# Kernel optimization log

Hardware: AMD Instinct MI355X
Metric: run time of the kernel (lower is better)

## Reference

```python
import jax, jax.numpy as jnp
import numpy as np

D = 768
H = 12
DH = D // H
PAIRS4 = [(0, 1), (0, 2), (0, 3), (1, 2), (1, 3), (2, 3)]
J6 = jnp.array([[0,0,0,0,0,1],[0,0,0,0,-1,0],[0,0,0,1,0,0],[0,0,1,0,0,0],[0,-1,0,0,0,0],[1,0,0,0,0,0]], dtype=jnp.float32)


def exterior(p1, p2):
    # p1,p2: (..., 4) -> normalized Plucker coords (..., 6)
    parts = [p1[..., i] * p2[..., j] - p1[..., j] * p2[..., i] for i, j in PAIRS4]
    L = jnp.stack(parts, axis=-1)
    n = jnp.clip(jnp.linalg.norm(L, axis=-1, keepdims=True), 1e-12)
    return L / n


def layernorm(x, g, b, eps=1e-5):
    m = jnp.mean(x, axis=-1, keepdims=True)
    v = jnp.var(x, axis=-1, keepdims=True)
    return (x - m) * jax.lax.rsqrt(v + eps) * g + b


def setup_inputs() -> dict:
    key = jax.random.key(0)
    ks = jax.random.split(key, 16)
    s = 0.02
    inp = {
        'x': jax.random.normal(ks[0], (1, 2048, D), dtype=jnp.float32),
        'ln1_g': jnp.ones((D,), jnp.float32), 'ln1_b': jnp.zeros((D,), jnp.float32),
        'qkv_w': jax.random.normal(ks[1], (D, 3 * D), jnp.float32) * s,
        'qkv_b': jnp.zeros((3 * D,), jnp.float32),
        'w1_write': jax.random.normal(ks[2], (D, 4 * H), jnp.float32) * s,
        'w2_write': jax.random.normal(ks[3], (D, 4 * H), jnp.float32) * s,
        'w1_read': jax.random.normal(ks[4], (D, 4 * H), jnp.float32) * s,
        'w2_read': jax.random.normal(ks[5], (D, 4 * H), jnp.float32) * s,
        'geo_v_w': jax.random.normal(ks[6], (D, D), jnp.float32) * s,
        'geo_v_b': jnp.zeros((D,), jnp.float32),
        'gate_w': jax.random.normal(ks[7], (D, H), jnp.float32) * s,
        'gate_b': jnp.zeros((H,), jnp.float32),
        'inc_scale': jnp.ones((H,), jnp.float32),
        'out_w': jax.random.normal(ks[8], (D, D), jnp.float32) * s,
        'out_b': jnp.zeros((D,), jnp.float32),
        'ln2_g': jnp.ones((D,), jnp.float32), 'ln2_b': jnp.zeros((D,), jnp.float32),
        'fc_w': jax.random.normal(ks[9], (D, 4 * D), jnp.float32) * s,
        'fc_b': jnp.zeros((4 * D,), jnp.float32),
        'proj_w': jax.random.normal(ks[10], (4 * D, D), jnp.float32) * s,
        'proj_b': jnp.zeros((D,), jnp.float32),
    }
    return inp


def dual_path_attention(x, qkv_w, qkv_b, w1_write, w2_write, w1_read, w2_read,
                        geo_v_w, geo_v_b, gate_w, gate_b, inc_scale, out_w, out_b):
    B, T, _ = x.shape
    scale = DH ** -0.5
    qkv = (x @ qkv_w + qkv_b).reshape(B, T, 3, H, DH)
    q = qkv[:, :, 0].transpose(0, 2, 1, 3)  # (B,H,T,dh)
    k = qkv[:, :, 1].transpose(0, 2, 1, 3)
    v = qkv[:, :, 2].transpose(0, 2, 1, 3)
    std_logits = jnp.einsum('bhtd,bhsd->bhts', q, k) * scale

    x_prev = jnp.concatenate([jnp.zeros((B, 1, x.shape[-1]), x.dtype), x[:, :-1]], axis=1)
    w1 = (x_prev @ w1_write).reshape(B, T, H, 4)
    w2 = (x @ w2_write).reshape(B, T, H, 4)
    write_lines = exterior(w1, w2)  # (B,T,H,6)
    r1 = (x @ w1_read).reshape(B, T, H, 4)
    r2 = (x @ w2_read).reshape(B, T, H, 4)
    read_lines = exterior(r1, r2)
    J_write = jnp.einsum('bthi,ij->bthj', write_lines, J6)
    geo_logits = jnp.einsum('bthp,bshp->bhts', read_lines, J_write)
    geo_logits = geo_logits * inc_scale[None, :, None, None]

    mask = jnp.triu(jnp.ones((T, T), dtype=bool), k=1)  # True above diagonal
    neg = jnp.finfo(x.dtype).min
    std_attn = jax.nn.softmax(jnp.where(mask, neg, std_logits), axis=-1)
    std_out = jnp.einsum('bhts,bhsd->bthd', std_attn, v).reshape(B, T, -1)
    geo_attn = jax.nn.softmax(jnp.where(mask, neg, geo_logits), axis=-1)
    geo_v = (x @ geo_v_w + geo_v_b).reshape(B, T, H, DH).transpose(0, 2, 1, 3)
    geo_out = jnp.einsum('bhts,bhsd->bthd', geo_attn, geo_v).reshape(B, T, -1)

    gate = jax.nn.sigmoid(x @ gate_w + gate_b).mean(axis=-1, keepdims=True)
    combined = (1 - gate) * std_out + gate * geo_out
    return combined @ out_w + out_b


def reference(x, ln1_g, ln1_b, qkv_w, qkv_b, w1_write, w2_write, w1_read, w2_read,
              geo_v_w, geo_v_b, gate_w, gate_b, inc_scale, out_w, out_b,
              ln2_g, ln2_b, fc_w, fc_b, proj_w, proj_b):
    h = x + dual_path_attention(layernorm(x, ln1_g, ln1_b), qkv_w, qkv_b,
                                w1_write, w2_write, w1_read, w2_read,
                                geo_v_w, geo_v_b, gate_w, gate_b, inc_scale,
                                out_w, out_b)
    m = layernorm(h, ln2_g, ln2_b)
    mlp = jax.nn.gelu(m @ fc_w + fc_b) @ proj_w + proj_b
    return h + mlp
```

## Files before the change

kernel.cpp:

```cpp
#include <hip/hip_runtime.h>
#include <hip/hip_bf16.h>
#include <math.h>

#define TT 2048
#define DD 768

typedef __bf16 bf16x8 __attribute__((ext_vector_type(8)));
typedef float f32x4 __attribute__((ext_vector_type(4)));

__device__ __forceinline__ void gload16(const void* g, void* l) {
    __builtin_amdgcn_global_load_lds(
        (const __attribute__((address_space(1))) unsigned int*)g,
        (__attribute__((address_space(3))) unsigned int*)l, 16, 0, 0);
}

__device__ __forceinline__ bf16x8 zero8() {
    bf16x8 v;
    #pragma unroll
    for (int j = 0; j < 8; ++j) v[j] = (__bf16)0.0f;
    return v;
}

__global__ __launch_bounds__(256) void ln_kernel(const float* __restrict__ in,
    const float* __restrict__ g, const float* __restrict__ b,
    __hip_bfloat16* __restrict__ out)
{
    const int t = blockIdx.x;
    const int tid = threadIdx.x;
    const float* row = in + (size_t)t * DD;
    float x0 = row[tid], x1 = row[tid + 256], x2 = row[tid + 512];
    float s = x0 + x1 + x2;
    float q = x0 * x0 + x1 * x1 + x2 * x2;
    #pragma unroll
    for (int m = 1; m < 64; m <<= 1) {
        s += __shfl_xor(s, m);
        q += __shfl_xor(q, m);
    }
    __shared__ float ssum[4], sqsum[4];
    const int w = tid >> 6;
    if ((tid & 63) == 0) { ssum[w] = s; sqsum[w] = q; }
    __syncthreads();
    s = ssum[0] + ssum[1] + ssum[2] + ssum[3];
    q = sqsum[0] + sqsum[1] + sqsum[2] + sqsum[3];
    const float mean = s * (1.0f / DD);
    const float var = q * (1.0f / DD) - mean * mean;
    const float rs = rsqrtf(var + 1e-5f);
    __hip_bfloat16* orow = out + (size_t)t * DD;
    orow[tid]       = __float2bfloat16((x0 - mean) * rs * g[tid]       + b[tid]);
    orow[tid + 256] = __float2bfloat16((x1 - mean) * rs * g[tid + 256] + b[tid + 256]);
    orow[tid + 512] = __float2bfloat16((x2 - mean) * rs * g[tid + 512] + b[tid + 512]);
}

__global__ __launch_bounds__(256) void castT_kernel(const float* __restrict__ in,
    __hip_bfloat16* __restrict__ out, int K, int N)
{
    __shared__ float t[32][33];
    const int n0 = blockIdx.x << 5, k0 = blockIdx.y << 5;
    const int tx = threadIdx.x & 31, ty = threadIdx.x >> 5;
    #pragma unroll
    for (int i = 0; i < 32; i += 8)
        t[ty + i][tx] = in[(size_t)(k0 + ty + i) * N + n0 + tx];
    __syncthreads();
    #pragma unroll
    for (int i = 0; i < 32; i += 8)
        out[(size_t)(n0 + ty + i) * K + k0 + tx] = __float2bfloat16(t[tx][ty + i]);
}

__device__ __forceinline__ float gelu_f(float x) {
    float u = 0.7978845608028654f * (x + 0.044715f * x * x * x);
    return 0.5f * x * (1.0f + tanhf(u));
}

__global__ __launch_bounds__(256) void mgemm64_kernel(
    const __hip_bfloat16* __restrict__ A, const __hip_bfloat16* __restrict__ Bt,
    const float* __restrict__ bias, const float* __restrict__ resid,
    void* __restrict__ Cout, float* __restrict__ Pb0, float* __restrict__ Pb1,
    int M, int N, int K, int kz, int epi, int omode)
{
    __shared__ __hip_bfloat16 As[64 * 32];
    __shared__ __hip_bfloat16 Bs[128 * 32];
    const int tid = threadIdx.x;
    const int lane = tid & 63, w = tid >> 6;
    const int colBase = blockIdx.x << 7, rowBase = blockIdx.y << 6;
    const int z = blockIdx.z;
    const int Kc = K / kz, koff = z * Kc;

    const int lr = lane >> 2, pc = lane & 3;
    const int n = lane & 15, quad = lane >> 4;

    const int arow = (w << 4) + lr;
    const int ac = (pc ^ ((arow >> 1) & 3)) << 3;
    const int brow0 = (w << 5) + lr, brow1 = brow0 + 16;
    const int bc0 = (pc ^ ((brow0 >> 1) & 3)) << 3;
    const int bc1 = (pc ^ ((brow1 >> 1) & 3)) << 3;

    f32x4 acc[8];
    #pragma unroll
    for (int j = 0; j < 8; ++j) acc[j] = (f32x4){0.f, 0.f, 0.f, 0.f};

    const int arF = (w << 4) + n;
    const int aposF = (quad ^ ((arF >> 1) & 3)) << 3;

    for (int kk = koff; kk < koff + Kc; kk += 32) {
        __syncthreads();
        gload16(A  + (size_t)(rowBase + arow) * K + kk + ac,   &As[(w << 4) * 32]);
        gload16(Bt + (size_t)(colBase + brow0) * K + kk + bc0, &Bs[(w << 5) * 32]);
        gload16(Bt + (size_t)(colBase + brow1) * K + kk + bc1, &Bs[((w << 5) + 16) * 32]);
        __syncthreads();

        bf16x8 af = *(const bf16x8*)&As[arF * 32 + aposF];
        #pragma unroll
        for (int j = 0; j < 8; ++j) {
            const int rb = (j << 4) + n;
            bf16x8 bfj = *(const bf16x8*)&Bs[rb * 32 + ((quad ^ ((rb >> 1) & 3)) << 3)];
            acc[j] = __builtin_amdgcn_mfma_f32_16x16x32_bf16(af, bfj, acc[j], 0, 0, 0);
        }
    }

    if (kz == 1) {
        #pragma unroll
        for (int j = 0; j < 8; ++j) {
            const int col = colBase + (j << 4) + n;
            const float bj = bias[col];
            #pragma unroll
            for (int r = 0; r < 4; ++r) {
                const int row = rowBase + (w << 4) + (quad << 2) + r;
                float v = acc[j][r] + bj;
                if (epi == 1) v = gelu_f(v);
                else if (epi == 2) v += resid[(size_t)row * N + col];
                if (omode == 1) ((__hip_bfloat16*)Cout)[(size_t)row * N + col] = __float2bfloat16(v);
                else ((float*)Cout)[(size_t)row * N + col] = v;
            }
        }
    } else {
        float* P = (z == 0) ? Pb0 : Pb1;
        #pragma unroll
        for (int j = 0; j < 8; ++j) {
            const int col = colBase + (j << 4) + n;
            #pragma unroll
            for (int r = 0; r < 4; ++r) {
                const int row = rowBase + (w << 4) + (quad << 2) + r;
                P[(size_t)row * N + col] = acc[j][r];
            }
        }
    }
}

__global__ __launch_bounds__(256) void kred_kernel(
    const float* __restrict__ p0, const float* __restrict__ p1,
    const float* __restrict__ bias, const float* __restrict__ resid,
    float* __restrict__ out, int N)
{
    const int base = (blockIdx.x * 256 + threadIdx.x) << 2;
    float4 a = *(const float4*)&p0[base];
    float4 b = *(const float4*)&p1[base];
    float4 bi = *(const float4*)&bias[base % N];
    float4 rs = *(const float4*)&resid[base];
    float4 o;
    o.x = a.x + b.x + bi.x + rs.x;
    o.y = a.y + b.y + bi.y + rs.y;
    o.z = a.z + b.z + bi.z + rs.z;
    o.w = a.w + b.w + bi.w + rs.w;
    *(float4*)&out[base] = o;
}

__device__ __forceinline__ void exterior6(const float* a, const float* b, float* L) {
    L[0] = a[0] * b[1] - a[1] * b[0];
    L[1] = a[0] * b[2] - a[2] * b[0];
    L[2] = a[0] * b[3] - a[3] * b[0];
    L[3] = a[1] * b[2] - a[2] * b[1];
    L[4] = a[1] * b[3] - a[3] * b[1];
    L[5] = a[2] * b[3] - a[3] * b[2];
    float n = sqrtf(L[0]*L[0] + L[1]*L[1] + L[2]*L[2] + L[3]*L[3] + L[4]*L[4] + L[5]*L[5]);
    float inv = 1.f / fmaxf(n, 1e-12f);
    #pragma unroll
    for (int p = 0; p < 6; ++p) L[p] *= inv;
}

__global__ __launch_bounds__(256) void smallproj_kernel(
    const __hip_bfloat16* __restrict__ ln1,
    const float* __restrict__ w1w, const float* __restrict__ w2w,
    const float* __restrict__ w1r, const float* __restrict__ w2r,
    const float* __restrict__ gw, const float* __restrict__ gb,
    __hip_bfloat16* __restrict__ rlb, __hip_bfloat16* __restrict__ jwb,
    float* __restrict__ gate)
{
    const int t = blockIdx.x;
    const int tid = threadIdx.x;
    __shared__ float xc[768], xp[768], res[204];
    const __hip_bfloat16* cur = ln1 + (size_t)t * DD;
    #pragma unroll
    for (int i = 0; i < 3; ++i) {
        int idx = tid + (i << 8);
        xc[idx] = __bfloat162float(cur[idx]);
        xp[idx] = (t > 0) ? __bfloat162float(cur[idx - DD]) : 0.f;
    }
    __syncthreads();
    if (tid < 204) {
        const float* wsel; const float* xv; int col, stride;
        if (tid < 48)       { wsel = w2w; xv = xc; col = tid;       stride = 48; }
        else if (tid < 96)  { wsel = w1w; xv = xp; col = tid - 48;  stride = 48; }
        else if (tid < 144) { wsel = w1r; xv = xc; col = tid - 96;  stride = 48; }
        else if (tid < 192) { wsel = w2r; xv = xc; col = tid - 144; stride = 48; }
        else                { wsel = gw;  xv = xc; col = tid - 192; stride = 12; }
        float s = 0.f;
        for (int k = 0; k < 768; ++k) s += xv[k] * wsel[(size_t)k * stride + col];
        if (tid >= 192) s += gb[col];
        res[tid] = s;
    }
    __syncthreads();
    if (tid < 12) {
        const int h = tid;
        float a[4], b[4], L[6];
        #pragma unroll
        for (int i = 0; i < 4; ++i) { a[i] = res[48 + h * 4 + i]; b[i] = res[h * 4 + i]; }
        exterior6(a, b, L);
        __hip_bfloat16* jwp = jwb + (size_t)h * 16384 + t * 8;
        jwp[0] = __float2bfloat16( L[5]); jwp[1] = __float2bfloat16(-L[4]);
        jwp[2] = __float2bfloat16( L[3]); jwp[3] = __float2bfloat16( L[2]);
        jwp[4] = __float2bfloat16(-L[1]); jwp[5] = __float2bfloat16( L[0]);
        jwp[6] = __float2bfloat16(0.f);   jwp[7] = __float2bfloat16(0.f);
        #pragma unroll
        for (int i = 0; i < 4; ++i) { a[i] = res[96 + h * 4 + i]; b[i] = res[144 + h * 4 + i]; }
        exterior6(a, b, L);
        __hip_bfloat16* rlp = rlb + (size_t)h * 16384 + t * 8;
        #pragma unroll
        for (int p = 0; p < 6; ++p) rlp[p] = __float2bfloat16(L[p]);
        rlp[6] = __float2bfloat16(0.f); rlp[7] = __float2bfloat16(0.f);
    }
    if (tid == 0) {
        float g = 0.f;
        #pragma unroll
        for (int i = 0; i < 12; ++i) g += 1.f / (1.f + __expf(-res[192 + i]));
        gate[t] = g * (1.f / 12.f);
    }
}

__global__ __launch_bounds__(256) void vt_kernel(
    const __hip_bfloat16* __restrict__ qkvB, const __hip_bfloat16* __restrict__ geovB,
    __hip_bfloat16* __restrict__ VT, __hip_bfloat16* __restrict__ GVT)
{
    __shared__ __hip_bfloat16 tile[64][72];
    const int s0 = blockIdx.x << 6, h = blockIdx.y;
    const bool isGV = (blockIdx.z != 0);
    const __hip_bfloat16* src = isGV ? (geovB + h * 64) : (qkvB + 1536 + h * 64);
    const int stride = isGV ? 768 : 2304;
    __hip_bfloat16* dst = (isGV ? GVT : VT) + (size_t)h * 131072;
    const int tid = threadIdx.x;
    const int r = tid >> 2, c = (tid & 3) << 3;
    *(bf16x8*)&tile[r][c]      = *(const bf16x8*)&src[(size_t)(s0 + r) * stride + c];
    *(bf16x8*)&tile[r][c + 32] = *(const bf16x8*)&src[(size_t)(s0 + r) * stride + c + 32];
    __syncthreads();
    __hip_bfloat16 tmp[8];
    #pragma unroll
    for (int j = 0; j < 8; ++j) tmp[j] = tile[c + j][r];
    *(bf16x8*)&dst[(size_t)r * 2048 + s0 + c] = *(const bf16x8*)tmp;
    #pragma unroll
    for (int j = 0; j < 8; ++j) tmp[j] = tile[c + 32 + j][r];
    *(bf16x8*)&dst[(size_t)r * 2048 + s0 + c + 32] = *(const bf16x8*)tmp;
}

__global__ __launch_bounds__(256) void mattn_kernel(
    const __hip_bfloat16* __restrict__ qkvB, const __hip_bfloat16* __restrict__ VT,
    const __hip_bfloat16* __restrict__ GVT, const __hip_bfloat16* __restrict__ rlb,
    const __hip_bfloat16* __restrict__ jwb, const float* __restrict__ gate,
    const float* __restrict__ inc_scale, __hip_bfloat16* __restrict__ comb,
    __hip_bfloat16* __restrict__ Opart, float* __restrict__ stats)
{
    __shared__ __hip_bfloat16 Ks0[2048], Ks1[2048];
    __shared__ __hip_bfloat16 VTs0[2048], VTs1[2048];
    __shared__ __hip_bfloat16 GVTs0[2048], GVTs1[2048];
    __shared__ __hip_bfloat16 JWs[64][8];
    __shared__ __bf16 Ps[64][72];
    __shared__ __bf16 Pg[64][72];

    const int j = 59 - blockIdx.x;
    const int hh = blockIdx.y;
    int qt, c, nc;
    if (j < 12)      { qt = j; c = 0; nc = 1; }
    else if (j < 36) { int t2 = j - 12; qt = 12 + (t2 >> 1); c = t2 & 1; nc = 2; }
    else             { int t2 = j - 36; int d3 = t2 / 3; qt = 24 + d3; c = t2 - d3 * 3; nc = 3; }
    const int q0 = qt << 6;
    const int nk = qt + 1;
    const int ktb = c * nk / nc;
    const int kte = (c + 1) * nk / nc - 1;
    const int tid = threadIdx.x;
    const int w = tid >> 6, lane = tid & 63;
    const int n = lane & 15, quad = lane >> 4;

    const int qrow = q0 + (w << 4) + n;
    const size_t qb = (size_t)qrow * 2304 + hh * 64;
    bf16x8 af0 = *(const bf16x8*)&qkvB[qb + (quad << 3)];
    bf16x8 af1 = *(const bf16x8*)&qkvB[qb + 32 + (quad << 3)];
    bf16x8 rlA = zero8();
    if (quad == 0) rlA = *(const bf16x8*)&rlb[(size_t)hh * 16384 + (size_t)qrow * 8];
    const float isc = inc_scale[hh];
    const float mgc = fabsf(isc);
    const size_t vbase = (size_t)hh * 131072;

    const int sRow = tid >> 2, sc = tid & 3;
    const int sPos = ((sc ^ ((sRow >> 1) & 3)) << 3);
    const int sOff = sc << 3;

    f32x4 Os[4], Og[4];
    float m_s[4], lsp[4], lgp[4];
    #pragma unroll
    for (int r = 0; r < 4; ++r) {
        m_s[r] = -1e30f; lsp[r] = 0.f; lgp[r] = 0.f;
        Os[r] = (f32x4){0.f, 0.f, 0.f, 0.f};
        Og[r] = (f32x4){0.f, 0.f, 0.f, 0.f};
    }

    bf16x8 rK0, rK1, rV0, rV1, rG0, rG1, rJ = zero8();
    {
        const int k0 = ktb << 6;
        const size_t kb = (size_t)(k0 + sRow) * 2304 + 768 + hh * 64;
        const size_t vb = vbase + (size_t)sRow * 2048 + k0;
        rK0 = *(const bf16x8*)&qkvB[kb + sOff];
        rK1 = *(const bf16x8*)&qkvB[kb + sOff + 32];
        rV0 = *(const bf16x8*)&VT[vb + sOff];
        rV1 = *(const bf16x8*)&VT[vb + sOff + 32];
        rG0 = *(const bf16x8*)&GVT[vb + sOff];
        rG1 = *(const bf16x8*)&GVT[vb + sOff + 32];
        if (tid < 64) rJ = *(const bf16x8*)&jwb[(size_t)hh * 16384 + (size_t)(k0 + tid) * 8];
    }

    for (int kt = ktb; kt <= kte; ++kt) {
        const int k0 = kt << 6;
        __syncthreads();
        *(bf16x8*)&Ks0[sRow * 32 + sPos]  = rK0;
        *(bf16x8*)&Ks1[sRow * 32 + sPos]  = rK1;
        *(bf16x8*)&VTs0[sRow * 32 + sPos] = rV0;
        *(bf16x8*)&VTs1[sRow * 32 + sPos] = rV1;
        *(bf16x8*)&GVTs0[sRow * 32 + sPos] = rG0;
        *(bf16x8*)&GVTs1[sRow * 32 + sPos] = rG1;
        if (tid < 64) *(bf16x8*)&JWs[tid][0] = rJ;
        if (kt < kte) {
            const int k1 = (kt + 1) << 6;
            const size_t kb = (size_t)(k1 + sRow) * 2304 + 768 + hh * 64;
            const size_t vb = vbase + (size_t)sRow * 2048 + k1;
            rK0 = *(const bf16x8*)&qkvB[kb + sOff];
            rK1 = *(const bf16x8*)&qkvB[kb + sOff + 32];
            rV0 = *(const bf16x8*)&VT[vb + sOff];
            rV1 = *(const bf16x8*)&VT[vb + sOff + 32];
            rG0 = *(const bf16x8*)&GVT[vb + sOff];
            rG1 = *(const bf16x8*)&GVT[vb + sOff + 32];
            if (tid < 64) rJ = *(const bf16x8*)&jwb[(size_t)hh * 16384 + (size_t)(k1 + tid) * 8];
        }
        __syncthreads();

        f32x4 Ss[4], Sg[4];
        #pragma unroll
        for (int t = 0; t < 4; ++t) {
            Ss[t] = (f32x4){0.f, 0.f, 0.f, 0.f};
            Sg[t] = (f32x4){0.f, 0.f, 0.f, 0.f};
        }
        #pragma unroll
        for (int t = 0; t < 4; ++t) {
            const int krow = (t << 4) + n;
            const int kpos = ((quad ^ ((krow >> 1) & 3)) << 3);
            bf16x8 kb0 = *(const bf16x8*)&Ks0[krow * 32 + kpos];
            bf16x8 kb1 = *(const bf16x8*)&Ks1[krow * 32 + kpos];
            Ss[t] = __builtin_amdgcn_mfma_f32_16x16x32_bf16(af0, kb0, Ss[t], 0, 0, 0);
            Ss[t] = __builtin_amdgcn_mfma_f32_16x16x32_bf16(af1, kb1, Ss[t], 0, 0, 0);
            bf16x8 jb = zero8();
            if (quad == 0) jb = *(const bf16x8*)&JWs[krow][0];
            Sg[t] = __builtin_amdgcn_mfma_f32_16x16x32_bf16(rlA, jb, Sg[t], 0, 0, 0);
        }
        #pragma unroll
        for (int t = 0; t < 4; ++t) {
            #pragma unroll
            for (int r = 0; r < 4; ++r) { Ss[t][r] *= 0.125f; Sg[t][r] *= isc; }
        }
        if (kt == qt) {
            #pragma unroll
            for (int t = 0; t < 4; ++t) {
                const int sg = k0 + (t << 4) + n;
                #pragma unroll
                for (int r = 0; r < 4; ++r) {
                    const int qg = q0 + (w << 4) + (quad << 2) + r;
                    if (sg > qg) { Ss[t][r] = -1e30f; Sg[t][r] = -1e30f; }
                }
            }
        }

        #pragma unroll
        for (int r = 0; r < 4; ++r) {
            float mx = fmaxf(fmaxf(Ss[0][r], Ss[1][r]), fmaxf(Ss[2][r], Ss[3][r]));
            #pragma unroll
            for (int mk = 1; mk < 16; mk <<= 1) mx = fmaxf(mx, __shfl_xor(mx, mk));
            float mnew = fmaxf(m_s[r], mx);
            float alpha = __expf(m_s[r] - mnew);
            m_s[r] = mnew;
            float sm = 0.f;
            #pragma unroll
            for (int t = 0; t < 4; ++t) { Ss[t][r] = __expf(Ss[t][r] - mnew); sm += Ss[t][r]; }
            lsp[r] = lsp[r] * alpha + sm;
            #pragma unroll
            for (int t = 0; t < 4; ++t) Os[t][r] *= alpha;

            float smg = 0.f;
            #pragma unroll
            for (int t = 0; t < 4; ++t) { Sg[t][r] = __expf(Sg[t][r] - mgc); smg += Sg[t][r]; }
            lgp[r] += smg;
        }

        #pragma unroll
        for (int t = 0; t < 4; ++t) {
            #pragma unroll
            for (int r = 0; r < 4; ++r) {
                Ps[(w << 4) + (quad << 2) + r][(t << 4) + n] = (__bf16)Ss[t][r];
                Pg[(w << 4) + (quad << 2) + r][(t << 4) + n] = (__bf16)Sg[t][r];
            }
        }
        asm volatile("s_waitcnt lgkmcnt(0)" ::: "memory");

        #pragma unroll
        for (int st = 0; st < 2; ++st) {
            bf16x8 ap = *(const bf16x8*)&Ps[(w << 4) + n][(st << 5) + (quad << 3)];
            bf16x8 gp = *(const bf16x8*)&Pg[(w << 4) + n][(st << 5) + (quad << 3)];
            const __hip_bfloat16* Vh = st ? VTs1 : VTs0;
            const __hip_bfloat16* Gh = st ? GVTs1 : GVTs0;
            #pragma unroll
            for (int dt = 0; dt < 4; ++dt) {
                const int vrow = (dt << 4) + n;
                const int vpos = ((quad ^ ((vrow >> 1) & 3)) << 3);
                bf16x8 vb2 = *(const bf16x8*)&Vh[vrow * 32 + vpos];
                bf16x8 gb2 = *(const bf16x8*)&Gh[vrow * 32 + vpos];
                Os[dt] = __builtin_amdgcn_mfma_f32_16x16x32_bf16(ap, vb2, Os[dt], 0, 0, 0);
                Og[dt] = __builtin_amdgcn_mfma_f32_16x16x32_bf16(gp, gb2, Og[dt], 0, 0, 0);
            }
        }
    }

    float l_s[4], l_g[4];
    #pragma unroll
    for (int r = 0; r < 4; ++r) {
        float ls = lsp[r], lg = lgp[r];
        #pragma unroll
        for (int mk = 1; mk < 16; mk <<= 1) {
            ls += __shfl_xor(ls, mk);
            lg += __shfl_xor(lg, mk);
        }
        l_s[r] = ls; l_g[r] = lg;
    }

    if (nc == 1) {
        #pragma unroll
        for (int r = 0; r < 4; ++r) {
            const int row = q0 + (w << 4) + (quad << 2) + r;
            const float g = gate[row];
            const float invs = (1.f - g) / l_s[r], invg = g / l_g[r];
            #pragma unroll
            for (int dt = 0; dt < 4; ++dt) {
                float val = Os[dt][r] * invs + Og[dt][r] * invg;
                comb[(size_t)row * DD + hh * 64 + (dt << 4) + n] = __float2bfloat16(val);
            }
        }
    } else {
        const int base = (qt < 24) ? ((qt - 12) << 1) : (24 + (qt - 24) * 3);
        const int slot = hh * 48 + base + c;
        __hip_bfloat16* op = Opart + (size_t)slot * 8192;
        float* st = stats + (size_t)slot * 256;
        #pragma unroll
        for (int r = 0; r < 4; ++r) {
            const int rloc = (w << 4) + (quad << 2) + r;
            #pragma unroll
            for (int dt = 0; dt < 4; ++dt) {
                const int col = (dt << 4) + n;
                op[rloc * 128 + col]      = __float2bfloat16(Os[dt][r]);
                op[rloc * 128 + 64 + col] = __float2bfloat16(Og[dt][r]);
            }
            if (n == 0) {
                st[rloc * 4 + 0] = m_s[r]; st[rloc * 4 + 1] = l_s[r];
                st[rloc * 4 + 2] = mgc;    st[rloc * 4 + 3] = l_g[r];
            }
        }
    }
}

__global__ __launch_bounds__(256) void acomb_kernel(
    const __hip_bfloat16* __restrict__ Opart, const float* __restrict__ stats,
    const float* __restrict__ gate, __hip_bfloat16* __restrict__ comb)
{
    const int qt = 12 + blockIdx.x;
    const int h = blockIdx.y;
    const int nc = (qt < 24) ? 2 : 3;
    const int sb = h * 48 + ((qt < 24) ? ((qt - 12) << 1) : (24 + (qt - 24) * 3));
    const int tid = threadIdx.x;
    const int rloc = tid >> 2;
    const int cseg = (tid & 3) << 4;
    const int row = (qt << 6) + rloc;
    float ms = -1e30f, mg = -1e30f;
    for (int c = 0; c < nc; ++c) {
        const float* st = stats + (size_t)(sb + c) * 256 + rloc * 4;
        ms = fmaxf(ms, st[0]);
        mg = fmaxf(mg, st[2]);
    }
    float wsc[3], wgc[3];
    float ls = 0.f, lg = 0.f;
    for (int c = 0; c < nc; ++c) {
        const float* st = stats + (size_t)(sb + c) * 256 + rloc * 4;
        wsc[c] = __expf(st[0] - ms); ls += st[1] * wsc[c];
        wgc[c] = __expf(st[2] - mg); lg += st[3] * wgc[c];
    }
    const float g = gate[row];
    const float fs = (1.f - g) / ls, fg = g / lg;
    #pragma unroll
    for (int cc = 0; cc < 16; ++cc) {
        const int col = cseg + cc;
        float os = 0.f, og = 0.f;
        for (int c = 0; c < nc; ++c) {
            const __hip_bfloat16* op = Opart + (size_t)(sb + c) * 8192 + rloc * 128;
            os += __bfloat162float(op[col]) * wsc[c];
            og += __bfloat162float(op[64 + col]) * wgc[c];
        }
        comb[(size_t)row * DD + h * 64 + col] = __float2bfloat16(os * fs + og * fg);
    }
}

extern "C" void kernel_launch(void* const* d_in, const int* in_sizes, int n_in,
                              void* d_out, int out_size, void* d_ws, size_t ws_size,
                              hipStream_t stream) {
    (void)in_sizes; (void)n_in; (void)out_size; (void)ws_size;
    const float* x      = (const float*)d_in[0];
    const float* ln1_g  = (const float*)d_in[1];
    const float* ln1_b  = (const float*)d_in[2];
    const float* qkv_w  = (const float*)d_in[3];
    const float* qkv_b  = (const float*)d_in[4];
    const float* w1w    = (const float*)d_in[5];
    const float* w2w    = (const float*)d_in[6];
    const float* w1r    = (const float*)d_in[7];
    const float* w2r    = (const float*)d_in[8];
    const float* gvw    = (const float*)d_in[9];
    const float* gvb    = (const float*)d_in[10];
    const float* gw     = (const float*)d_in[11];
    const float* gb     = (const float*)d_in[12];
    const float* isc    = (const float*)d_in[13];
    const float* ow     = (const float*)d_in[14];
    const float* ob     = (const float*)d_in[15];
    const float* ln2_g  = (const float*)d_in[16];
    const float* ln2_b  = (const float*)d_in[17];
    const float* fcw    = (const float*)d_in[18];
    const float* fcb    = (const float*)d_in[19];
    const float* pw     = (const float*)d_in[20];
    const float* pb     = (const float*)d_in[21];
    float* out = (float*)d_out;
    char* wsb  = (char*)d_ws;

    __hip_bfloat16* qkvB  = (__hip_bfloat16*)(wsb + 0);
    __hip_bfloat16* geovB = (__hip_bfloat16*)(wsb + 9437184);
    __hip_bfloat16* VTb   = (__hip_bfloat16*)(wsb + 12582912);
    __hip_bfloat16* GVTb  = (__hip_bfloat16*)(wsb + 15728640);
    __hip_bfloat16* rlb   = (__hip_bfloat16*)(wsb + 18874368);
    __hip_bfloat16* jwb   = (__hip_bfloat16*)(wsb + 19267584);
    float*          gate  = (float*)(wsb + 19660800);
    __hip_bfloat16* ln1   = (__hip_bfloat16*)(wsb + 19668992);
    __hip_bfloat16* comb  = (__hip_bfloat16*)(wsb + 22814720);
    float*          hbuf  = (float*)(wsb + 25960448);
    __hip_bfloat16* qkvwt = (__hip_bfloat16*)(wsb + 32251904);
    __hip_bfloat16* gvwt  = (__hip_bfloat16*)(wsb + 35790848);
    __hip_bfloat16* owt   = (__hip_bfloat16*)(wsb + 36970496);
    float*          stats = (float*)(wsb + 38150144);
    __hip_bfloat16* Opart = (__hip_bfloat16*)hbuf;
    __hip_bfloat16* fcwt  = qkvwt;
    __hip_bfloat16* pwt   = (__hip_bfloat16*)(wsb + 0);
    __hip_bfloat16* fcact = (__hip_bfloat16*)(wsb + 4718592);
    float* Ppart0 = (float*)(wsb + 18874368);
    float* Ppart1 = (float*)(wsb + 32251904);

    castT_kernel<<<dim3(72, 24), 256, 0, stream>>>(qkv_w, qkvwt, 768, 2304);
    castT_kernel<<<dim3(24, 24), 256, 0, stream>>>(gvw, gvwt, 768, 768);
    ln_kernel<<<TT, 256, 0, stream>>>(x, ln1_g, ln1_b, ln1);
    mgemm64_kernel<<<dim3(18, 32, 1), 256, 0, stream>>>(ln1, qkvwt, qkv_b, nullptr, qkvB, nullptr, nullptr, TT, 2304, 768, 1, 0, 1);
    mgemm64_kernel<<<dim3(6, 32, 1), 256, 0, stream>>>(ln1, gvwt, gvb, nullptr, geovB, nullptr, nullptr, TT, 768, 768, 1, 0, 1);
    vt_kernel<<<dim3(32, 12, 2), 256, 0, stream>>>(qkvB, geovB, VTb, GVTb);
    smallproj_kernel<<<TT, 256, 0, stream>>>(ln1, w1w, w2w, w1r, w2r, gw, gb, rlb, jwb, gate);
    mattn_kernel<<<dim3(60, 12), 256, 0, stream>>>(qkvB, VTb, GVTb, rlb, jwb, gate, isc, comb, Opart, stats);
    acomb_kernel<<<dim3(20, 12), 256, 0, stream>>>(Opart, stats, gate, comb);
    castT_kernel<<<dim3(24, 24), 256, 0, stream>>>(ow, owt, 768, 768);
    mgemm64_kernel<<<dim3(6, 32, 1), 256, 0, stream>>>(comb, owt, ob, x, hbuf, nullptr, nullptr, TT, 768, 768, 1, 2, 0);
    ln_kernel<<<TT, 256, 0, stream>>>(hbuf, ln2_g, ln2_b, ln1);
    castT_kernel<<<dim3(96, 24), 256, 0, stream>>>(fcw, fcwt, 768, 3072);
    mgemm64_kernel<<<dim3(24, 32, 1), 256, 0, stream>>>(ln1, fcwt, fcb, nullptr, fcact, nullptr, nullptr, TT, 3072, 768, 1, 1, 1);
    castT_kernel<<<dim3(24, 96), 256, 0, stream>>>(pw, pwt, 3072, 768);
    mgemm64_kernel<<<dim3(6, 32, 2), 256, 0, stream>>>(fcact, pwt, pb, nullptr, nullptr, Ppart0, Ppart1, TT, 768, 3072, 2, 0, 0);
    kred_kernel<<<1536, 256, 0, stream>>>(Ppart0, Ppart1, pb, hbuf, out, 768);
}
```

Before: 392.1 us.

## Replace scalar small-projection kernel with concatenated-weight MFMA GEMM plus light epilogue

The per-token scalar dot-product kernel for the write/read/gate projections is replaced. The five small weight matrices are first packed, transposed, into one bf16 matrix padded to 256 rows. A bf16 MFMA GEMM then computes all projections for every token, and a small per-token kernel does the exterior products and the gate. The aim is to remove the slow strided fp32 scalar loop that reread the weights for each of the 2048 tokens. The cost is two extra launches, bf16 rounding of these weights, and the use of the uninitialized padding rows 204-255 in the GEMM.

```diff
diff --git a/kernel.cpp b/kernel.cpp
--- a/kernel.cpp
+++ b/kernel.cpp
@@ -66,6 +66,26 @@
         out[(size_t)(n0 + ty + i) * K + k0 + tx] = __float2bfloat16(t[tx][ty + i]);
 }
 
+__global__ __launch_bounds__(256) void wcat_kernel(
+    const float* __restrict__ w2w, const float* __restrict__ w1w,
+    const float* __restrict__ w1r, const float* __restrict__ w2r,
+    const float* __restrict__ gw, __hip_bfloat16* __restrict__ Wcat)
+{
+    const int nrow = blockIdx.x;
+    const float* src; int col, stride;
+    if (nrow < 48)       { src = w2w; col = nrow;       stride = 48; }
+    else if (nrow < 96)  { src = w1w; col = nrow - 48;  stride = 48; }
+    else if (nrow < 144) { src = w1r; col = nrow - 96;  stride = 48; }
+    else if (nrow < 192) { src = w2r; col = nrow - 144; stride = 48; }
+    else                 { src = gw;  col = nrow - 192; stride = 12; }
+    const int tid = threadIdx.x;
+    #pragma unroll
+    for (int i = 0; i < 3; ++i) {
+        const int k = tid + (i << 8);
+        Wcat[(size_t)nrow * 768 + k] = __float2bfloat16(src[(size_t)k * stride + col]);
+    }
+}
+
 __device__ __forceinline__ float gelu_f(float x) {
     float u = 0.7978845608028654f * (x + 0.044715f * x * x * x);
     return 0.5f * x * (1.0f + tanhf(u));
@@ -121,7 +141,7 @@
         #pragma unroll
         for (int j = 0; j < 8; ++j) {
             const int col = colBase + (j << 4) + n;
-            const float bj = bias[col];
+            const float bj = bias ? bias[col] : 0.f;
             #pragma unroll
             for (int r = 0; r < 4; ++r) {
                 const int row = rowBase + (w << 4) + (quad << 2) + r;
@@ -177,43 +197,22 @@
     for (int p = 0; p < 6; ++p) L[p] *= inv;
 }
 
-__global__ __launch_bounds__(256) void smallproj_kernel(
-    const __hip_bfloat16* __restrict__ ln1,
-    const float* __restrict__ w1w, const float* __restrict__ w2w,
-    const float* __restrict__ w1r, const float* __restrict__ w2r,
-    const float* __restrict__ gw, const float* __restrict__ gb,
+__global__ __launch_bounds__(64) void extgate_kernel(
+    const float* __restrict__ P, const float* __restrict__ gb,
     __hip_bfloat16* __restrict__ rlb, __hip_bfloat16* __restrict__ jwb,
     float* __restrict__ gate)
 {
     const int t = blockIdx.x;
     const int tid = threadIdx.x;
-    __shared__ float xc[768], xp[768], res[204];
-    const __hip_bfloat16* cur = ln1 + (size_t)t * DD;
-    #pragma unroll
-    for (int i = 0; i < 3; ++i) {
-        int idx = tid + (i << 8);
-        xc[idx] = __bfloat162float(cur[idx]);
-        xp[idx] = (t > 0) ? __bfloat162float(cur[idx - DD]) : 0.f;
-    }
-    __syncthreads();
-    if (tid < 204) {
-        const float* wsel; const float* xv; int col, stride;
-        if (tid < 48)       { wsel = w2w; xv = xc; col = tid;       stride = 48; }
-        else if (tid < 96)  { wsel = w1w; xv = xp; col = tid - 48;  stride = 48; }
-        else if (tid < 144) { wsel = w1r; xv = xc; col = tid - 96;  stride = 48; }
-        else if (tid < 192) { wsel = w2r; xv = xc; col = tid - 144; stride = 48; }
-        else                { wsel = gw;  xv = xc; col = tid - 192; stride = 12; }
-        float s = 0.f;
-        for (int k = 0; k < 768; ++k) s += xv[k] * wsel[(size_t)k * stride + col];
-        if (tid >= 192) s += gb[col];
-        res[tid] = s;
-    }
-    __syncthreads();
+    const float* row = P + (size_t)t * 256;
     if (tid < 12) {
         const int h = tid;
         float a[4], b[4], L[6];
         #pragma unroll
-        for (int i = 0; i < 4; ++i) { a[i] = res[48 + h * 4 + i]; b[i] = res[h * 4 + i]; }
+        for (int i = 0; i < 4; ++i) {
+            a[i] = (t > 0) ? row[-256 + 48 + h * 4 + i] : 0.f;
+            b[i] = row[h * 4 + i];
+        }
         exterior6(a, b, L);
         __hip_bfloat16* jwp = jwb + (size_t)h * 16384 + t * 8;
         jwp[0] = __float2bfloat16( L[5]); jwp[1] = __float2bfloat16(-L[4]);
@@ -221,17 +220,17 @@
         jwp[4] = __float2bfloat16(-L[1]); jwp[5] = __float2bfloat16( L[0]);
         jwp[6] = __float2bfloat16(0.f);   jwp[7] = __float2bfloat16(0.f);
         #pragma unroll
-        for (int i = 0; i < 4; ++i) { a[i] = res[96 + h * 4 + i]; b[i] = res[144 + h * 4 + i]; }
+        for (int i = 0; i < 4; ++i) { a[i] = row[96 + h * 4 + i]; b[i] = row[144 + h * 4 + i]; }
         exterior6(a, b, L);
         __hip_bfloat16* rlp = rlb + (size_t)h * 16384 + t * 8;
         #pragma unroll
         for (int p = 0; p < 6; ++p) rlp[p] = __float2bfloat16(L[p]);
         rlp[6] = __float2bfloat16(0.f); rlp[7] = __float2bfloat16(0.f);
     }
-    if (tid == 0) {
+    if (tid == 32) {
         float g = 0.f;
         #pragma unroll
-        for (int i = 0; i < 12; ++i) g += 1.f / (1.f + __expf(-res[192 + i]));
+        for (int i = 0; i < 12; ++i) g += 1.f / (1.f + __expf(-(row[192 + i] + gb[i])));
         gate[t] = g * (1.f / 12.f);
     }
 }
@@ -568,14 +567,18 @@
     __hip_bfloat16* fcact = (__hip_bfloat16*)(wsb + 4718592);
     float* Ppart0 = (float*)(wsb + 18874368);
     float* Ppart1 = (float*)(wsb + 32251904);
+    __hip_bfloat16* Wcat  = owt;
+    float*          Pproj = (float*)(wsb + 22814720);
 
     castT_kernel<<<dim3(72, 24), 256, 0, stream>>>(qkv_w, qkvwt, 768, 2304);
     castT_kernel<<<dim3(24, 24), 256, 0, stream>>>(gvw, gvwt, 768, 768);
+    wcat_kernel<<<204, 256, 0, stream>>>(w2w, w1w, w1r, w2r, gw, Wcat);
     ln_kernel<<<TT, 256, 0, stream>>>(x, ln1_g, ln1_b, ln1);
+    mgemm64_kernel<<<dim3(2, 32, 1), 256, 0, stream>>>(ln1, Wcat, nullptr, nullptr, Pproj, nullptr, nullptr, TT, 256, 768, 1, 0, 0);
+    extgate_kernel<<<TT, 64, 0, stream>>>(Pproj, gb, rlb, jwb, gate);
     mgemm64_kernel<<<dim3(18, 32, 1), 256, 0, stream>>>(ln1, qkvwt, qkv_b, nullptr, qkvB, nullptr, nullptr, TT, 2304, 768, 1, 0, 1);
     mgemm64_kernel<<<dim3(6, 32, 1), 256, 0, stream>>>(ln1, gvwt, gvb, nullptr, geovB, nullptr, nullptr, TT, 768, 768, 1, 0, 1);
     vt_kernel<<<dim3(32, 12, 2), 256, 0, stream>>>(qkvB, geovB, VTb, GVTb);
-    smallproj_kernel<<<TT, 256, 0, stream>>>(ln1, w1w, w2w, w1r, w2r, gw, gb, rlb, jwb, gate);
     mattn_kernel<<<dim3(60, 12), 256, 0, stream>>>(qkvB, VTb, GVTb, rlb, jwb, gate, isc, comb, Opart, stats);
     acomb_kernel<<<dim3(20, 12), 256, 0, stream>>>(Opart, stats, gate, comb);
     castT_kernel<<<dim3(24, 24), 256, 0, stream>>>(ow, owt, 768, 768);
```

New measurement: 357.0 us. 1.1x faster.
